# Performance work log

Hardware: AMD Instinct MI355X
Metric: run time of the kernel (lower is better)

The kernel has to match this reference:

```python
import jax, jax.numpy as jnp
import numpy as np

NUM_POS = 4
N = 8192
C = 4096  # number of identity classes == logit dim


def setup_inputs() -> dict:
    key = jax.random.key(0)
    k1, k2 = jax.random.split(key)
    feat = jax.random.normal(k1, (N, C), dtype=jnp.float32)
    label = jax.random.randint(k2, (N,), 0, C, dtype=jnp.int64)
    return {"feat": feat, "label": label}


def reference(feat, label):
    # feat: [n, C] logits, label: [n] int class ids.
    n, c = feat.shape
    # Segment-mean replaces the O(n^2) masked-mean loop:
    # center[i] = mean of feat over all j with label[j] == label[i]
    sums = jax.ops.segment_sum(feat, label, num_segments=c)              # [C, C]
    counts = jax.ops.segment_sum(jnp.ones((n,), feat.dtype), label,
                                 num_segments=c)                          # [C]
    center = sums[label] / counts[label][:, None]                         # [n, C]
    # CrossEntropyLoss (mean reduction) on centers as logits
    logp = jax.nn.log_softmax(center, axis=-1)
    ce = -jnp.take_along_axis(logp, label[:, None], axis=1)[:, 0].mean()
    m = n / NUM_POS
    return ce / m
```

## Files before the change

### kernel.cpp

```cpp
#include <hip/hip_runtime.h>
#include <math.h>

#define NN 8192
#define CC 4096
#define SLOTS 64
#define BLK 256

#define SCALE (4.0f / (8192.0f * 8192.0f))

__global__ void init_kernel(int* __restrict__ counts, float* __restrict__ out) {
    int i = blockIdx.x * blockDim.x + threadIdx.x;
    if (i < CC) counts[i] = 0;
    if (i == 0) out[0] = 0.0f;
}

__global__ void build_index(const int* __restrict__ label,
                            int* __restrict__ counts,
                            int* __restrict__ lists) {
    int i = blockIdx.x * blockDim.x + threadIdx.x;
    if (i < NN) {
        int lab = label[i];
        int pos = atomicAdd(&counts[lab], 1);
        if (pos < SLOTS) lists[lab * SLOTS + pos] = i;
    }
}

__global__ __launch_bounds__(BLK) void class_loss(const float* __restrict__ feat,
                                                  const int* __restrict__ counts,
                                                  const int* __restrict__ lists,
                                                  float* __restrict__ out) {
    int c = blockIdx.x;
    int cnt = counts[c];
    if (cnt == 0) return;

    int t = threadIdx.x;
    float4 acc[4];
    #pragma unroll
    for (int j = 0; j < 4; ++j) acc[j] = make_float4(0.f, 0.f, 0.f, 0.f);

    int m = cnt < SLOTS ? cnt : SLOTS;
    for (int k = 0; k < m; ++k) {
        int r = lists[c * SLOTS + k];
        const float4* rowp = (const float4*)(feat + (size_t)r * CC);
        #pragma unroll
        for (int j = 0; j < 4; ++j) {
            float4 v = rowp[j * 256 + t];
            acc[j].x += v.x; acc[j].y += v.y; acc[j].z += v.z; acc[j].w += v.w;
        }
    }

    float inv = 1.0f / (float)cnt;
    float vals[16];
    #pragma unroll
    for (int j = 0; j < 4; ++j) {
        vals[j * 4 + 0] = acc[j].x * inv;
        vals[j * 4 + 1] = acc[j].y * inv;
        vals[j * 4 + 2] = acc[j].z * inv;
        vals[j * 4 + 3] = acc[j].w * inv;
    }

    __shared__ float s_red[4];
    __shared__ float s_bcast;
    __shared__ float s_vc;

    float wm = vals[0];
    #pragma unroll
    for (int j = 1; j < 16; ++j) wm = fmaxf(wm, vals[j]);
    #pragma unroll
    for (int off = 32; off > 0; off >>= 1) wm = fmaxf(wm, __shfl_down(wm, off, 64));
    int lane = t & 63, wv = t >> 6;
    if (lane == 0) s_red[wv] = wm;
    __syncthreads();
    if (t == 0) s_bcast = fmaxf(fmaxf(s_red[0], s_red[1]), fmaxf(s_red[2], s_red[3]));
    __syncthreads();
    float M = s_bcast;

    float se = 0.f;
    #pragma unroll
    for (int j = 0; j < 16; ++j) se += expf(vals[j] - M);
    #pragma unroll
    for (int off = 32; off > 0; off >>= 1) se += __shfl_down(se, off, 64);
    if (lane == 0) s_red[wv] = se;

    if (t == ((c & 1023) >> 2)) s_vc = vals[((c >> 10) << 2) | (c & 3)];
    __syncthreads();

    if (t == 0) {
        float S = s_red[0] + s_red[1] + s_red[2] + s_red[3];
        float value = M + logf(S) - s_vc;
        atomicAdd(out, (float)cnt * value * SCALE);
    }
}

extern "C" void kernel_launch(void* const* d_in, const int* in_sizes, int n_in,
                              void* d_out, int out_size, void* d_ws, size_t ws_size,
                              hipStream_t stream) {
    const float* feat = (const float*)d_in[0];
    const int* label = (const int*)d_in[1];
    float* out = (float*)d_out;

    int* counts = (int*)d_ws;
    int* lists = counts + CC;

    init_kernel<<<(CC + BLK - 1) / BLK, BLK, 0, stream>>>(counts, out);
    build_index<<<(NN + BLK - 1) / BLK, BLK, 0, stream>>>(label, counts, lists);
    class_loss<<<CC, BLK, 0, stream>>>(feat, counts, lists, out);
}
```

Measured before the change: 205.3 us.

## Split per-class softmax into wave-level column chunks with a separate finalize pass

Each class's logsumexp is now split across 16 column chunks, and each chunk is handled by one wavefront instead of a whole block. Partial (max, sum-exp, target logit) triples are written to a workspace. A new finalize kernel merges them with an online logsumexp and reduces the loss. The gather of member rows is batched up front, with templated unrolls, to raise memory-level parallelism. This removes the block-level syncthreads and increases the number of independent work items. The cost is an extra kernel launch and the partial-buffer traffic, and fast exp/log intrinsics replace the precise ones.

Result: faster. 201.1 us (-2.0%).

```diff
diff --git a/kernel.cpp b/kernel.cpp
--- a/kernel.cpp
+++ b/kernel.cpp
@@ -5,6 +5,7 @@
 #define CC 4096
 #define SLOTS 64
 #define BLK 256
+#define NSPLIT 16
 
 #define SCALE (4.0f / (8192.0f * 8192.0f))
 
@@ -25,71 +26,103 @@
     }
 }
 
-__global__ __launch_bounds__(BLK) void class_loss(const float* __restrict__ feat,
-                                                  const int* __restrict__ counts,
-                                                  const int* __restrict__ lists,
-                                                  float* __restrict__ out) {
-    int c = blockIdx.x;
+template <int T>
+__device__ inline float4 gather_sum(const float4* __restrict__ feat4,
+                                    const int* __restrict__ rl, int m, int slot) {
+    int r0 = rl[0];
+    float4 v[T];
+    #pragma unroll
+    for (int k = 0; k < T; ++k) {
+        int r = (k < m) ? rl[k] : r0;
+        v[k] = feat4[(size_t)r * (CC / 4) + slot];
+    }
+    float4 a = make_float4(0.f, 0.f, 0.f, 0.f);
+    #pragma unroll
+    for (int k = 0; k < T; ++k) {
+        float w = (k < m) ? 1.f : 0.f;
+        a.x += w * v[k].x; a.y += w * v[k].y; a.z += w * v[k].z; a.w += w * v[k].w;
+    }
+    return a;
+}
+
+__global__ __launch_bounds__(BLK) void part_kernel(const float4* __restrict__ feat4,
+                                                   const int* __restrict__ counts,
+                                                   const int* __restrict__ lists,
+                                                   float4* __restrict__ part) {
+    int lane = threadIdx.x & 63;
+    int wv = __builtin_amdgcn_readfirstlane(threadIdx.x >> 6);
+    int task = blockIdx.x * 4 + wv;
+    int c = task >> 4;
+    int s = task & 15;
+
     int cnt = counts[c];
     if (cnt == 0) return;
+    int m = cnt < SLOTS ? cnt : SLOTS;
 
-    int t = threadIdx.x;
-    float4 acc[4];
-    #pragma unroll
-    for (int j = 0; j < 4; ++j) acc[j] = make_float4(0.f, 0.f, 0.f, 0.f);
+    const int* rl = lists + c * SLOTS;
+    int slot = s * 64 + lane;
 
-    int m = cnt < SLOTS ? cnt : SLOTS;
-    for (int k = 0; k < m; ++k) {
-        int r = lists[c * SLOTS + k];
-        const float4* rowp = (const float4*)(feat + (size_t)r * CC);
-        #pragma unroll
-        for (int j = 0; j < 4; ++j) {
-            float4 v = rowp[j * 256 + t];
-            acc[j].x += v.x; acc[j].y += v.y; acc[j].z += v.z; acc[j].w += v.w;
+    float4 acc;
+    if (m <= 2)      acc = gather_sum<2>(feat4, rl, m, slot);
+    else if (m <= 4) acc = gather_sum<4>(feat4, rl, m, slot);
+    else if (m <= 8) acc = gather_sum<8>(feat4, rl, m, slot);
+    else {
+        acc = gather_sum<16>(feat4, rl, m, slot);
+        for (int k = 16; k < m; ++k) {
+            float4 v = feat4[(size_t)rl[k] * (CC / 4) + slot];
+            acc.x += v.x; acc.y += v.y; acc.z += v.z; acc.w += v.w;
         }
     }
 
     float inv = 1.0f / (float)cnt;
-    float vals[16];
+    float mean[4] = {acc.x * inv, acc.y * inv, acc.z * inv, acc.w * inv};
+
+    float M = fmaxf(fmaxf(mean[0], mean[1]), fmaxf(mean[2], mean[3]));
     #pragma unroll
-    for (int j = 0; j < 4; ++j) {
-        vals[j * 4 + 0] = acc[j].x * inv;
-        vals[j * 4 + 1] = acc[j].y * inv;
-        vals[j * 4 + 2] = acc[j].z * inv;
-        vals[j * 4 + 3] = acc[j].w * inv;
+    for (int off = 1; off < 64; off <<= 1) M = fmaxf(M, __shfl_xor(M, off, 64));
+
+    float S = __expf(mean[0] - M) + __expf(mean[1] - M) +
+              __expf(mean[2] - M) + __expf(mean[3] - M);
+    #pragma unroll
+    for (int off = 1; off < 64; off <<= 1) S += __shfl_xor(S, off, 64);
+
+    float cand = mean[c & 3];
+    float vcown = __shfl(cand, (c >> 2) & 63, 64);
+    float vc = (s == (c >> 8)) ? vcown : 0.f;
+
+    if (lane == 0) part[s * CC + c] = make_float4(M, S, vc, 0.f);
+}
+
+__global__ __launch_bounds__(BLK) void finalize(const float4* __restrict__ part,
+                                                const int* __restrict__ counts,
+                                                float* __restrict__ out) {
+    int c = blockIdx.x * BLK + threadIdx.x;
+    int cnt = counts[c];
+    float contrib = 0.f;
+    if (cnt > 0) {
+        float4 p[NSPLIT];
+        #pragma unroll
+        for (int s = 0; s < NSPLIT; ++s) p[s] = part[s * CC + c];
+        float M = p[0].x;
+        #pragma unroll
+        for (int s = 1; s < NSPLIT; ++s) M = fmaxf(M, p[s].x);
+        float S = 0.f, vc = 0.f;
+        #pragma unroll
+        for (int s = 0; s < NSPLIT; ++s) {
+            S += p[s].y * __expf(p[s].x - M);
+            vc += p[s].z;
+        }
+        contrib = (float)cnt * (M + __logf(S) - vc);
     }
 
+    #pragma unroll
+    for (int off = 1; off < 64; off <<= 1) contrib += __shfl_xor(contrib, off, 64);
     __shared__ float s_red[4];
-    __shared__ float s_bcast;
-    __shared__ float s_vc;
-
-    float wm = vals[0];
-    #pragma unroll
-    for (int j = 1; j < 16; ++j) wm = fmaxf(wm, vals[j]);
-    #pragma unroll
-    for (int off = 32; off > 0; off >>= 1) wm = fmaxf(wm, __shfl_down(wm, off, 64));
-    int lane = t & 63, wv = t >> 6;
-    if (lane == 0) s_red[wv] = wm;
+    int lane = threadIdx.x & 63, w = threadIdx.x >> 6;
+    if (lane == 0) s_red[w] = contrib;
     __syncthreads();
-    if (t == 0) s_bcast = fmaxf(fmaxf(s_red[0], s_red[1]), fmaxf(s_red[2], s_red[3]));
-    __syncthreads();
-    float M = s_bcast;
-
-    float se = 0.f;
-    #pragma unroll
-    for (int j = 0; j < 16; ++j) se += expf(vals[j] - M);
-    #pragma unroll
-    for (int off = 32; off > 0; off >>= 1) se += __shfl_down(se, off, 64);
-    if (lane == 0) s_red[wv] = se;
-
-    if (t == ((c & 1023) >> 2)) s_vc = vals[((c >> 10) << 2) | (c & 3)];
-    __syncthreads();
-
-    if (t == 0) {
-        float S = s_red[0] + s_red[1] + s_red[2] + s_red[3];
-        float value = M + logf(S) - s_vc;
-        atomicAdd(out, (float)cnt * value * SCALE);
-    }
+    if (threadIdx.x == 0)
+        atomicAdd(out, (s_red[0] + s_red[1] + s_red[2] + s_red[3]) * SCALE);
 }
 
 extern "C" void kernel_launch(void* const* d_in, const int* in_sizes, int n_in,
@@ -101,8 +134,10 @@
 
     int* counts = (int*)d_ws;
     int* lists = counts + CC;
+    float4* part = (float4*)(lists + CC * SLOTS);
 
     init_kernel<<<(CC + BLK - 1) / BLK, BLK, 0, stream>>>(counts, out);
     build_index<<<(NN + BLK - 1) / BLK, BLK, 0, stream>>>(label, counts, lists);
-    class_loss<<<CC, BLK, 0, stream>>>(feat, counts, lists, out);
+    part_kernel<<<CC * NSPLIT / 4, BLK, 0, stream>>>((const float4*)feat, counts, lists, part);
+    finalize<<<CC / BLK, BLK, 0, stream>>>(part, counts, out);
 }
```
